# Kernel optimization log

Measured on AMD Instinct MI355X. Metric: run time of the kernel, lower is better.

Reference implementation:

```python
import jax, jax.numpy as jnp
import numpy as np

D_MODEL = 1024
HEAD_SIZE = 64

def setup_inputs() -> dict:
    key = jax.random.key(0)
    ks = jax.random.split(key, 7)
    s = 1.0 / np.sqrt(D_MODEL)
    return {
        "x": jax.random.normal(ks[0], (4, 2048, D_MODEL), dtype=jnp.float32),
        "wq": jax.random.uniform(ks[1], (D_MODEL, HEAD_SIZE), jnp.float32, -s, s),
        "bq": jax.random.uniform(ks[2], (HEAD_SIZE,), jnp.float32, -s, s),
        "wk": jax.random.uniform(ks[3], (D_MODEL, HEAD_SIZE), jnp.float32, -s, s),
        "bk": jax.random.uniform(ks[4], (HEAD_SIZE,), jnp.float32, -s, s),
        "wv": jax.random.uniform(ks[5], (D_MODEL, HEAD_SIZE), jnp.float32, -s, s),
        "bv": jax.random.uniform(ks[6], (HEAD_SIZE,), jnp.float32, -s, s),
    }

def reference(x, wq, bq, wk, bk, wv, bv):
    # x: [b, n, d_model]; projections -> [b, n, head_size]
    q = x @ wq + bq
    k = x @ wk + bk
    v = x @ wv + bv
    scores = jnp.einsum("bnd,bmd->bnm", q, k) / jnp.sqrt(jnp.float32(HEAD_SIZE))
    attn = jax.nn.softmax(scores, axis=-1)  # [b, n, n]
    return jnp.einsum("bnm,bmd->bnd", attn, v)
```

## Files before the change

kernel.cpp:

```cpp
#include <hip/hip_runtime.h>
#include <math.h>

#define D_MODEL 1024
#define HEAD 64
#define SEQ 2048
#define BATCH 4

typedef _Float16 f16x4 __attribute__((ext_vector_type(4)));
typedef _Float16 f16x8 __attribute__((ext_vector_type(8)));
typedef float f32x4 __attribute__((ext_vector_type(4)));

__global__ __launch_bounds__(256) void prep_w(
    const float* __restrict__ wq, const float* __restrict__ wk,
    const float* __restrict__ wv, _Float16* __restrict__ wT)
{
    const float* w = (blockIdx.y == 0) ? wq : (blockIdx.y == 1) ? wk : wv;
    const int kbase = blockIdx.x * 64;
    __shared__ float t[64][65];
    const int tid = threadIdx.x;
    #pragma unroll
    for (int i = 0; i < 16; i++) {
        int idx = tid + i * 256;
        int kk = idx >> 6, c = idx & 63;
        t[kk][c] = w[(size_t)(kbase + kk) * 64 + c];
    }
    __syncthreads();
    #pragma unroll
    for (int i = 0; i < 16; i++) {
        int idx = tid + i * 256;
        int c = idx >> 6, kk = idx & 63;
        wT[(size_t)(blockIdx.y * 64 + c) * 1024 + kbase + kk] = (_Float16)t[kk][c];
    }
}

__global__ __launch_bounds__(768, 6) void proj_kernel(
    const float* __restrict__ x, const _Float16* __restrict__ wT,
    const float* __restrict__ bq, const float* __restrict__ bk2,
    const float* __restrict__ bv,
    _Float16* __restrict__ q, _Float16* __restrict__ k, _Float16* __restrict__ vT)
{
    const int tid = threadIdx.x;
    const int wave = tid >> 6;
    const int lane = tid & 63;
    const int l16 = lane & 15;
    const int quad = lane >> 4;
    const int row0 = blockIdx.x * 16;

    __shared__ __align__(16) _Float16 Xs[2][16][136];

    const int srow = tid >> 5;
    const int sc4 = tid & 31;
    const float4* xg = reinterpret_cast<const float4*>(x)
                     + (size_t)(row0 + srow) * (D_MODEL / 4) + sc4;

    const _Float16* wp = wT + (size_t)(wave * 16 + l16) * D_MODEL + quad * 8;

    float4 xr;
    if (tid < 512) {
        xr = xg[0];
        f16x4 h;
        h[0] = (_Float16)xr.x; h[1] = (_Float16)xr.y;
        h[2] = (_Float16)xr.z; h[3] = (_Float16)xr.w;
        *(f16x4*)&Xs[0][srow][sc4 * 4] = h;
    }

    f32x4 acc = (f32x4){0.f, 0.f, 0.f, 0.f};

    #pragma unroll 1
    for (int c = 0; c < 8; c++) {
        __syncthreads();
        f16x8 bw0 = *(const f16x8*)(wp + c * 128);
        f16x8 bw1 = *(const f16x8*)(wp + c * 128 + 32);
        f16x8 bw2 = *(const f16x8*)(wp + c * 128 + 64);
        f16x8 bw3 = *(const f16x8*)(wp + c * 128 + 96);
        if (c < 7 && tid < 512) xr = xg[(c + 1) * 32];
        const int bsel = c & 1;
        f16x8 aX0 = *(const f16x8*)&Xs[bsel][l16][0 * 32 + quad * 8];
        f16x8 aX1 = *(const f16x8*)&Xs[bsel][l16][1 * 32 + quad * 8];
        f16x8 aX2 = *(const f16x8*)&Xs[bsel][l16][2 * 32 + quad * 8];
        f16x8 aX3 = *(const f16x8*)&Xs[bsel][l16][3 * 32 + quad * 8];
        acc = __builtin_amdgcn_mfma_f32_16x16x32_f16(aX0, bw0, acc, 0, 0, 0);
        acc = __builtin_amdgcn_mfma_f32_16x16x32_f16(aX1, bw1, acc, 0, 0, 0);
        acc = __builtin_amdgcn_mfma_f32_16x16x32_f16(aX2, bw2, acc, 0, 0, 0);
        acc = __builtin_amdgcn_mfma_f32_16x16x32_f16(aX3, bw3, acc, 0, 0, 0);
        if (c < 7 && tid < 512) {
            f16x4 h;
            h[0] = (_Float16)xr.x; h[1] = (_Float16)xr.y;
            h[2] = (_Float16)xr.z; h[3] = (_Float16)xr.w;
            *(f16x4*)&Xs[bsel ^ 1][srow][sc4 * 4] = h;
        }
    }

    const int g = wave * 16 + l16;
    const int batch = row0 / SEQ;
    const int rbase = row0 + quad * 4;
    if (g < 64) {
        float bias = bq[g];
        #pragma unroll
        for (int r = 0; r < 4; r++)
            q[(size_t)(rbase + r) * HEAD + g] = (_Float16)((acc[r] + bias) * 0.125f);
    } else if (g < 128) {
        float bias = bk2[g - 64];
        #pragma unroll
        for (int r = 0; r < 4; r++)
            k[(size_t)(rbase + r) * HEAD + (g - 64)] = (_Float16)(acc[r] + bias);
    } else {
        float bias = bv[g - 128];
        f16x4 pk;
        #pragma unroll
        for (int r = 0; r < 4; r++) pk[r] = (_Float16)(acc[r] + bias);
        const int seq0 = row0 - batch * SEQ + quad * 4;
        *(f16x4*)(vT + (size_t)(batch * HEAD + (g - 128)) * SEQ + seq0) = pk;
    }
}

__global__ __launch_bounds__(512, 4) void attn_kernel(
    const _Float16* __restrict__ q, const _Float16* __restrict__ k,
    const _Float16* __restrict__ vT, float* __restrict__ out)
{
    const int tid = threadIdx.x;
    const int wave = tid >> 6;
    const int lane = tid & 63;
    const int l16 = lane & 15;
    const int quad = lane >> 4;
    const int b = blockIdx.y;
    const int q0 = blockIdx.x * 16;

    __shared__ __align__(16) char SM[2 * 18432 + 2 * 17408];
    _Float16 (*Ks)[128][72] = (_Float16(*)[128][72])SM;
    _Float16 (*Vs)[64][136] = (_Float16(*)[64][136])(SM + 2 * 18432);
    float (*Oall)[16][68] = (float(*)[16][68])SM;
    __shared__ float Lall[8][16];

    f16x8 bQ[2];
    {
        const _Float16* qp = q + (size_t)(b * SEQ + q0 + l16) * HEAD + quad * 8;
        bQ[0] = *(const f16x8*)qp;
        bQ[1] = *(const f16x8*)(qp + 32);
    }

    f32x4 O[4];
    #pragma unroll
    for (int dt = 0; dt < 4; dt++) O[dt] = (f32x4){0.f, 0.f, 0.f, 0.f};
    float lpart = 0.f;

    const _Float16* kb = k + (size_t)b * SEQ * HEAD;
    const _Float16* vb = vT + (size_t)b * HEAD * SEQ;

    const int krow = tid >> 3, kc8 = (tid & 7) * 8;
    const int vrow = tid >> 4, vc8 = (tid & 15) * 8;
    const _Float16* kg = kb + (size_t)krow * HEAD + kc8;
    const _Float16* vg = vb + (size_t)vrow * SEQ + vc8;

    f16x8 kr0 = *(const f16x8*)kg;
    f16x8 kr1 = *(const f16x8*)(kg + (size_t)64 * HEAD);
    f16x8 vr0 = *(const f16x8*)vg;
    f16x8 vr1 = *(const f16x8*)(vg + (size_t)32 * SEQ);
    *(f16x8*)&Ks[0][krow][kc8] = kr0;
    *(f16x8*)&Ks[0][krow + 64][kc8] = kr1;
    *(f16x8*)&Vs[0][vrow][vc8] = vr0;
    *(f16x8*)&Vs[0][vrow + 32][vc8] = vr1;

    #pragma unroll 1
    for (int c = 0; c < 16; c++) {
        __syncthreads();
        if (c < 15) {
            const int kc2 = (c + 1) * 128;
            kr0 = *(const f16x8*)(kg + (size_t)kc2 * HEAD);
            kr1 = *(const f16x8*)(kg + (size_t)(kc2 + 64) * HEAD);
            vr0 = *(const f16x8*)(vg + kc2);
            vr1 = *(const f16x8*)(vg + (size_t)32 * SEQ + kc2);
        }
        const int bsel = c & 1;
        f16x8 aK0 = *(const f16x8*)&Ks[bsel][wave * 16 + l16][quad * 8];
        f16x8 aK1 = *(const f16x8*)&Ks[bsel][wave * 16 + l16][32 + quad * 8];
        f32x4 st = __builtin_amdgcn_mfma_f32_16x16x32_f16(aK0, bQ[0], (f32x4){0.f, 0.f, 0.f, 0.f}, 0, 0, 0);
        st = __builtin_amdgcn_mfma_f32_16x16x32_f16(aK1, bQ[1], st, 0, 0, 0);

        float p0 = __expf(st[0]);
        float p1 = __expf(st[1]);
        float p2 = __expf(st[2]);
        float p3 = __expf(st[3]);
        lpart += (p0 + p1) + (p2 + p3);
        f16x4 bP;
        bP[0] = (_Float16)p0; bP[1] = (_Float16)p1;
        bP[2] = (_Float16)p2; bP[3] = (_Float16)p3;

        #pragma unroll
        for (int dt = 0; dt < 4; dt++) {
            f16x4 aV = *(const f16x4*)&Vs[bsel][dt * 16 + l16][wave * 16 + quad * 4];
            O[dt] = __builtin_amdgcn_mfma_f32_16x16x16f16(aV, bP, O[dt], 0, 0, 0);
        }
        if (c < 15) {
            *(f16x8*)&Ks[bsel ^ 1][krow][kc8] = kr0;
            *(f16x8*)&Ks[bsel ^ 1][krow + 64][kc8] = kr1;
            *(f16x8*)&Vs[bsel ^ 1][vrow][vc8] = vr0;
            *(f16x8*)&Vs[bsel ^ 1][vrow + 32][vc8] = vr1;
        }
    }
    __syncthreads();

    lpart += __shfl_xor(lpart, 16);
    lpart += __shfl_xor(lpart, 32);
    if (lane < 16) Lall[wave][l16] = lpart;
    #pragma unroll
    for (int dt = 0; dt < 4; dt++)
        #pragma unroll
        for (int r = 0; r < 4; r++)
            Oall[wave][l16][dt * 16 + quad * 4 + r] = O[dt][r];
    __syncthreads();

    {
        int qi = tid >> 5;
        int dd = (tid & 31) * 2;
        float L = 0.f, o0 = 0.f, o1 = 0.f;
        #pragma unroll
        for (int w = 0; w < 8; w++) {
            L += Lall[w][qi];
            o0 += Oall[w][qi][dd];
            o1 += Oall[w][qi][dd + 1];
        }
        float inv = 1.f / L;
        float2 res = make_float2(o0 * inv, o1 * inv);
        *(float2*)(out + (size_t)(b * SEQ + q0 + qi) * HEAD + dd) = res;
    }
}

extern "C" void kernel_launch(void* const* d_in, const int* in_sizes, int n_in,
                              void* d_out, int out_size, void* d_ws, size_t ws_size,
                              hipStream_t stream) {
    const float* x  = (const float*)d_in[0];
    const float* wq = (const float*)d_in[1];
    const float* bq = (const float*)d_in[2];
    const float* wk = (const float*)d_in[3];
    const float* bk = (const float*)d_in[4];
    const float* wv = (const float*)d_in[5];
    const float* bv = (const float*)d_in[6];
    float* out = (float*)d_out;

    const size_t proj_elems = (size_t)BATCH * SEQ * HEAD;
    _Float16* qh = (_Float16*)d_ws;
    _Float16* kh = qh + proj_elems;
    _Float16* vT = kh + proj_elems;
    _Float16* wT = vT + proj_elems;

    prep_w<<<dim3(16, 3), 256, 0, stream>>>(wq, wk, wv, wT);
    proj_kernel<<<dim3(BATCH * SEQ / 16), 768, 0, stream>>>(x, wT, bq, bk, bv, qh, kh, vT);
    attn_kernel<<<dim3(SEQ / 16, BATCH), 512, 0, stream>>>(qh, kh, vT, out);
}
```

Measured before the change: 122.3 us.

## Load K/V fragments straight from global into registers, dropping LDS staging

The attention kernel no longer stages shared K and V tiles in double-buffered LDS behind per-iteration barriers. Each wave now owns a contiguous 256-key slice and loads its MFMA operand fragments directly from global memory into registers, prefetching one step ahead. The intent is to remove barrier stalls and LDS traffic and to shrink shared memory so more blocks fit per CU. The cost is narrower, less coalesced global loads (8-byte V fragments spread over many rows), which lean on L2 hits, and only a one-step prefetch to hide latency. The final O write to LDS is also vectorised.

```diff
diff --git a/kernel.cpp b/kernel.cpp
--- a/kernel.cpp
+++ b/kernel.cpp
@@ -126,56 +126,47 @@
     const int b = blockIdx.y;
     const int q0 = blockIdx.x * 16;
 
-    __shared__ __align__(16) char SM[2 * 18432 + 2 * 17408];
-    _Float16 (*Ks)[128][72] = (_Float16(*)[128][72])SM;
-    _Float16 (*Vs)[64][136] = (_Float16(*)[64][136])(SM + 2 * 18432);
-    float (*Oall)[16][68] = (float(*)[16][68])SM;
+    __shared__ __align__(16) float Oall[8][16][68];
     __shared__ float Lall[8][16];
 
-    f16x8 bQ[2];
+    f16x8 bQ0, bQ1;
     {
         const _Float16* qp = q + (size_t)(b * SEQ + q0 + l16) * HEAD + quad * 8;
-        bQ[0] = *(const f16x8*)qp;
-        bQ[1] = *(const f16x8*)(qp + 32);
-    }
+        bQ0 = *(const f16x8*)qp;
+        bQ1 = *(const f16x8*)(qp + 32);
+    }
+
+    const _Float16* kp = k + (size_t)(b * SEQ + wave * 256 + l16) * HEAD + quad * 8;
+    const _Float16* vp = vT + (size_t)(b * HEAD + l16) * SEQ + wave * 256 + quad * 4;
 
     f32x4 O[4];
     #pragma unroll
     for (int dt = 0; dt < 4; dt++) O[dt] = (f32x4){0.f, 0.f, 0.f, 0.f};
     float lpart = 0.f;
 
-    const _Float16* kb = k + (size_t)b * SEQ * HEAD;
-    const _Float16* vb = vT + (size_t)b * HEAD * SEQ;
-
-    const int krow = tid >> 3, kc8 = (tid & 7) * 8;
-    const int vrow = tid >> 4, vc8 = (tid & 15) * 8;
-    const _Float16* kg = kb + (size_t)krow * HEAD + kc8;
-    const _Float16* vg = vb + (size_t)vrow * SEQ + vc8;
-
-    f16x8 kr0 = *(const f16x8*)kg;
-    f16x8 kr1 = *(const f16x8*)(kg + (size_t)64 * HEAD);
-    f16x8 vr0 = *(const f16x8*)vg;
-    f16x8 vr1 = *(const f16x8*)(vg + (size_t)32 * SEQ);
-    *(f16x8*)&Ks[0][krow][kc8] = kr0;
-    *(f16x8*)&Ks[0][krow + 64][kc8] = kr1;
-    *(f16x8*)&Vs[0][vrow][vc8] = vr0;
-    *(f16x8*)&Vs[0][vrow + 32][vc8] = vr1;
+    f16x8 ka0 = *(const f16x8*)kp;
+    f16x8 ka1 = *(const f16x8*)(kp + 32);
+    f16x4 va0 = *(const f16x4*)vp;
+    f16x4 va1 = *(const f16x4*)(vp + 16 * SEQ);
+    f16x4 va2 = *(const f16x4*)(vp + 32 * SEQ);
+    f16x4 va3 = *(const f16x4*)(vp + 48 * SEQ);
 
     #pragma unroll 1
-    for (int c = 0; c < 16; c++) {
-        __syncthreads();
-        if (c < 15) {
-            const int kc2 = (c + 1) * 128;
-            kr0 = *(const f16x8*)(kg + (size_t)kc2 * HEAD);
-            kr1 = *(const f16x8*)(kg + (size_t)(kc2 + 64) * HEAD);
-            vr0 = *(const f16x8*)(vg + kc2);
-            vr1 = *(const f16x8*)(vg + (size_t)32 * SEQ + kc2);
-        }
-        const int bsel = c & 1;
-        f16x8 aK0 = *(const f16x8*)&Ks[bsel][wave * 16 + l16][quad * 8];
-        f16x8 aK1 = *(const f16x8*)&Ks[bsel][wave * 16 + l16][32 + quad * 8];
-        f32x4 st = __builtin_amdgcn_mfma_f32_16x16x32_f16(aK0, bQ[0], (f32x4){0.f, 0.f, 0.f, 0.f}, 0, 0, 0);
-        st = __builtin_amdgcn_mfma_f32_16x16x32_f16(aK1, bQ[1], st, 0, 0, 0);
+    for (int cc = 0; cc < 16; cc++) {
+        f16x8 nk0, nk1;
+        f16x4 nv0, nv1, nv2, nv3;
+        if (cc < 15) {
+            const _Float16* kn = kp + (size_t)(cc + 1) * 16 * HEAD;
+            nk0 = *(const f16x8*)kn;
+            nk1 = *(const f16x8*)(kn + 32);
+            const _Float16* vn = vp + (cc + 1) * 16;
+            nv0 = *(const f16x4*)vn;
+            nv1 = *(const f16x4*)(vn + 16 * SEQ);
+            nv2 = *(const f16x4*)(vn + 32 * SEQ);
+            nv3 = *(const f16x4*)(vn + 48 * SEQ);
+        }
+        f32x4 st = __builtin_amdgcn_mfma_f32_16x16x32_f16(ka0, bQ0, (f32x4){0.f, 0.f, 0.f, 0.f}, 0, 0, 0);
+        st = __builtin_amdgcn_mfma_f32_16x16x32_f16(ka1, bQ1, st, 0, 0, 0);
 
         float p0 = __expf(st[0]);
         float p1 = __expf(st[1]);
@@ -186,28 +177,23 @@
         bP[0] = (_Float16)p0; bP[1] = (_Float16)p1;
         bP[2] = (_Float16)p2; bP[3] = (_Float16)p3;
 
-        #pragma unroll
-        for (int dt = 0; dt < 4; dt++) {
-            f16x4 aV = *(const f16x4*)&Vs[bsel][dt * 16 + l16][wave * 16 + quad * 4];
-            O[dt] = __builtin_amdgcn_mfma_f32_16x16x16f16(aV, bP, O[dt], 0, 0, 0);
-        }
-        if (c < 15) {
-            *(f16x8*)&Ks[bsel ^ 1][krow][kc8] = kr0;
-            *(f16x8*)&Ks[bsel ^ 1][krow + 64][kc8] = kr1;
-            *(f16x8*)&Vs[bsel ^ 1][vrow][vc8] = vr0;
-            *(f16x8*)&Vs[bsel ^ 1][vrow + 32][vc8] = vr1;
-        }
-    }
-    __syncthreads();
+        O[0] = __builtin_amdgcn_mfma_f32_16x16x16f16(va0, bP, O[0], 0, 0, 0);
+        O[1] = __builtin_amdgcn_mfma_f32_16x16x16f16(va1, bP, O[1], 0, 0, 0);
+        O[2] = __builtin_amdgcn_mfma_f32_16x16x16f16(va2, bP, O[2], 0, 0, 0);
+        O[3] = __builtin_amdgcn_mfma_f32_16x16x16f16(va3, bP, O[3], 0, 0, 0);
+
+        if (cc < 15) {
+            ka0 = nk0; ka1 = nk1;
+            va0 = nv0; va1 = nv1; va2 = nv2; va3 = nv3;
+        }
+    }
 
     lpart += __shfl_xor(lpart, 16);
     lpart += __shfl_xor(lpart, 32);
     if (lane < 16) Lall[wave][l16] = lpart;
     #pragma unroll
     for (int dt = 0; dt < 4; dt++)
-        #pragma unroll
-        for (int r = 0; r < 4; r++)
-            Oall[wave][l16][dt * 16 + quad * 4 + r] = O[dt][r];
+        *(f32x4*)&Oall[wave][l16][dt * 16 + quad * 4] = O[dt];
     __syncthreads();
 
     {
```

After: 150.5 us. 23.1% more time.

## Share K/V tiles across two query tiles per block and pad V transpose

Applied to the files above, without the earlier changes.

The attention kernel now runs 1024 threads per block covering 32 queries, split into two 16-query groups of 8 waves. Both groups share each staged K/V chunk in LDS, so global K/V loads per query are halved and each thread issues one load per chunk instead of two. The transposed V buffer gets a padded row stride of 2080 to reduce conflicts on strided accesses. The trade-off is larger blocks with more threads synchronising on every barrier, and a larger workspace layout.

```diff
diff --git a/kernel.cpp b/kernel.cpp
--- a/kernel.cpp
+++ b/kernel.cpp
@@ -5,6 +5,7 @@
 #define HEAD 64
 #define SEQ 2048
 #define BATCH 4
+#define VSTRIDE 2080
 
 typedef _Float16 f16x4 __attribute__((ext_vector_type(4)));
 typedef _Float16 f16x8 __attribute__((ext_vector_type(8)));
@@ -110,72 +111,68 @@
         #pragma unroll
         for (int r = 0; r < 4; r++) pk[r] = (_Float16)(acc[r] + bias);
         const int seq0 = row0 - batch * SEQ + quad * 4;
-        *(f16x4*)(vT + (size_t)(batch * HEAD + (g - 128)) * SEQ + seq0) = pk;
-    }
-}
-
-__global__ __launch_bounds__(512, 4) void attn_kernel(
+        *(f16x4*)(vT + (size_t)(batch * HEAD + (g - 128)) * VSTRIDE + seq0) = pk;
+    }
+}
+
+__global__ __launch_bounds__(1024, 4) void attn_kernel(
     const _Float16* __restrict__ q, const _Float16* __restrict__ k,
     const _Float16* __restrict__ vT, float* __restrict__ out)
 {
     const int tid = threadIdx.x;
     const int wave = tid >> 6;
+    const int qt = wave >> 3;
+    const int ws = wave & 7;
     const int lane = tid & 63;
     const int l16 = lane & 15;
     const int quad = lane >> 4;
     const int b = blockIdx.y;
-    const int q0 = blockIdx.x * 16;
+    const int q0 = blockIdx.x * 32 + qt * 16;
 
     __shared__ __align__(16) char SM[2 * 18432 + 2 * 17408];
     _Float16 (*Ks)[128][72] = (_Float16(*)[128][72])SM;
     _Float16 (*Vs)[64][136] = (_Float16(*)[64][136])(SM + 2 * 18432);
     float (*Oall)[16][68] = (float(*)[16][68])SM;
-    __shared__ float Lall[8][16];
-
-    f16x8 bQ[2];
+    __shared__ float Lall[16][16];
+
+    f16x8 bQ0, bQ1;
     {
         const _Float16* qp = q + (size_t)(b * SEQ + q0 + l16) * HEAD + quad * 8;
-        bQ[0] = *(const f16x8*)qp;
-        bQ[1] = *(const f16x8*)(qp + 32);
-    }
-
-    f32x4 O[4];
-    #pragma unroll
-    for (int dt = 0; dt < 4; dt++) O[dt] = (f32x4){0.f, 0.f, 0.f, 0.f};
+        bQ0 = *(const f16x8*)qp;
+        bQ1 = *(const f16x8*)(qp + 32);
+    }
+
+    f32x4 O0 = {0.f, 0.f, 0.f, 0.f};
+    f32x4 O1 = {0.f, 0.f, 0.f, 0.f};
+    f32x4 O2 = {0.f, 0.f, 0.f, 0.f};
+    f32x4 O3 = {0.f, 0.f, 0.f, 0.f};
     float lpart = 0.f;
 
     const _Float16* kb = k + (size_t)b * SEQ * HEAD;
-    const _Float16* vb = vT + (size_t)b * HEAD * SEQ;
+    const _Float16* vb = vT + (size_t)b * HEAD * VSTRIDE;
 
     const int krow = tid >> 3, kc8 = (tid & 7) * 8;
     const int vrow = tid >> 4, vc8 = (tid & 15) * 8;
     const _Float16* kg = kb + (size_t)krow * HEAD + kc8;
-    const _Float16* vg = vb + (size_t)vrow * SEQ + vc8;
-
-    f16x8 kr0 = *(const f16x8*)kg;
-    f16x8 kr1 = *(const f16x8*)(kg + (size_t)64 * HEAD);
-    f16x8 vr0 = *(const f16x8*)vg;
-    f16x8 vr1 = *(const f16x8*)(vg + (size_t)32 * SEQ);
-    *(f16x8*)&Ks[0][krow][kc8] = kr0;
-    *(f16x8*)&Ks[0][krow + 64][kc8] = kr1;
-    *(f16x8*)&Vs[0][vrow][vc8] = vr0;
-    *(f16x8*)&Vs[0][vrow + 32][vc8] = vr1;
+    const _Float16* vg = vb + (size_t)vrow * VSTRIDE + vc8;
+
+    f16x8 kr = *(const f16x8*)kg;
+    f16x8 vr = *(const f16x8*)vg;
+    *(f16x8*)&Ks[0][krow][kc8] = kr;
+    *(f16x8*)&Vs[0][vrow][vc8] = vr;
 
     #pragma unroll 1
     for (int c = 0; c < 16; c++) {
         __syncthreads();
         if (c < 15) {
-            const int kc2 = (c + 1) * 128;
-            kr0 = *(const f16x8*)(kg + (size_t)kc2 * HEAD);
-            kr1 = *(const f16x8*)(kg + (size_t)(kc2 + 64) * HEAD);
-            vr0 = *(const f16x8*)(vg + kc2);
-            vr1 = *(const f16x8*)(vg + (size_t)32 * SEQ + kc2);
+            kr = *(const f16x8*)(kg + (size_t)(c + 1) * 128 * HEAD);
+            vr = *(const f16x8*)(vg + (c + 1) * 128);
         }
         const int bsel = c & 1;
-        f16x8 aK0 = *(const f16x8*)&Ks[bsel][wave * 16 + l16][quad * 8];
-        f16x8 aK1 = *(const f16x8*)&Ks[bsel][wave * 16 + l16][32 + quad * 8];
-        f32x4 st = __builtin_amdgcn_mfma_f32_16x16x32_f16(aK0, bQ[0], (f32x4){0.f, 0.f, 0.f, 0.f}, 0, 0, 0);
-        st = __builtin_amdgcn_mfma_f32_16x16x32_f16(aK1, bQ[1], st, 0, 0, 0);
+        f16x8 aK0 = *(const f16x8*)&Ks[bsel][ws * 16 + l16][quad * 8];
+        f16x8 aK1 = *(const f16x8*)&Ks[bsel][ws * 16 + l16][32 + quad * 8];
+        f32x4 st = __builtin_amdgcn_mfma_f32_16x16x32_f16(aK0, bQ0, (f32x4){0.f, 0.f, 0.f, 0.f}, 0, 0, 0);
+        st = __builtin_amdgcn_mfma_f32_16x16x32_f16(aK1, bQ1, st, 0, 0, 0);
 
         float p0 = __expf(st[0]);
         float p1 = __expf(st[1]);
@@ -186,16 +183,18 @@
         bP[0] = (_Float16)p0; bP[1] = (_Float16)p1;
         bP[2] = (_Float16)p2; bP[3] = (_Float16)p3;
 
-        #pragma unroll
-        for (int dt = 0; dt < 4; dt++) {
-            f16x4 aV = *(const f16x4*)&Vs[bsel][dt * 16 + l16][wave * 16 + quad * 4];
-            O[dt] = __builtin_amdgcn_mfma_f32_16x16x16f16(aV, bP, O[dt], 0, 0, 0);
-        }
+        f16x4 aV0 = *(const f16x4*)&Vs[bsel][0 * 16 + l16][ws * 16 + quad * 4];
+        f16x4 aV1 = *(const f16x4*)&Vs[bsel][1 * 16 + l16][ws * 16 + quad * 4];
+        f16x4 aV2 = *(const f16x4*)&Vs[bsel][2 * 16 + l16][ws * 16 + quad * 4];
+        f16x4 aV3 = *(const f16x4*)&Vs[bsel][3 * 16 + l16][ws * 16 + quad * 4];
+        O0 = __builtin_amdgcn_mfma_f32_16x16x16f16(aV0, bP, O0, 0, 0, 0);
+        O1 = __builtin_amdgcn_mfma_f32_16x16x16f16(aV1, bP, O1, 0, 0, 0);
+        O2 = __builtin_amdgcn_mfma_f32_16x16x16f16(aV2, bP, O2, 0, 0, 0);
+        O3 = __builtin_amdgcn_mfma_f32_16x16x16f16(aV3, bP, O3, 0, 0, 0);
+
         if (c < 15) {
-            *(f16x8*)&Ks[bsel ^ 1][krow][kc8] = kr0;
-            *(f16x8*)&Ks[bsel ^ 1][krow + 64][kc8] = kr1;
-            *(f16x8*)&Vs[bsel ^ 1][vrow][vc8] = vr0;
-            *(f16x8*)&Vs[bsel ^ 1][vrow + 32][vc8] = vr1;
+            *(f16x8*)&Ks[bsel ^ 1][krow][kc8] = kr;
+            *(f16x8*)&Vs[bsel ^ 1][vrow][vc8] = vr;
         }
     }
     __syncthreads();
@@ -203,26 +202,27 @@
     lpart += __shfl_xor(lpart, 16);
     lpart += __shfl_xor(lpart, 32);
     if (lane < 16) Lall[wave][l16] = lpart;
-    #pragma unroll
-    for (int dt = 0; dt < 4; dt++)
-        #pragma unroll
-        for (int r = 0; r < 4; r++)
-            Oall[wave][l16][dt * 16 + quad * 4 + r] = O[dt][r];
+    *(f32x4*)&Oall[wave][l16][0 * 16 + quad * 4] = O0;
+    *(f32x4*)&Oall[wave][l16][1 * 16 + quad * 4] = O1;
+    *(f32x4*)&Oall[wave][l16][2 * 16 + quad * 4] = O2;
+    *(f32x4*)&Oall[wave][l16][3 * 16 + quad * 4] = O3;
     __syncthreads();
 
     {
         int qi = tid >> 5;
         int dd = (tid & 31) * 2;
+        int wbase = (qi >> 4) * 8;
+        int qr = qi & 15;
         float L = 0.f, o0 = 0.f, o1 = 0.f;
         #pragma unroll
         for (int w = 0; w < 8; w++) {
-            L += Lall[w][qi];
-            o0 += Oall[w][qi][dd];
-            o1 += Oall[w][qi][dd + 1];
+            L += Lall[wbase + w][qr];
+            o0 += Oall[wbase + w][qr][dd];
+            o1 += Oall[wbase + w][qr][dd + 1];
         }
         float inv = 1.f / L;
         float2 res = make_float2(o0 * inv, o1 * inv);
-        *(float2*)(out + (size_t)(b * SEQ + q0 + qi) * HEAD + dd) = res;
+        *(float2*)(out + (size_t)(b * SEQ + blockIdx.x * 32 + qi) * HEAD + dd) = res;
     }
 }
 
@@ -242,9 +242,9 @@
     _Float16* qh = (_Float16*)d_ws;
     _Float16* kh = qh + proj_elems;
     _Float16* vT = kh + proj_elems;
-    _Float16* wT = vT + proj_elems;
+    _Float16* wT = vT + (size_t)BATCH * HEAD * VSTRIDE;
 
     prep_w<<<dim3(16, 3), 256, 0, stream>>>(wq, wk, wv, wT);
     proj_kernel<<<dim3(BATCH * SEQ / 16), 768, 0, stream>>>(x, wT, bq, bk, bv, qh, kh, vT);
-    attn_kernel<<<dim3(SEQ / 16, BATCH), 512, 0, stream>>>(qh, kh, vT, out);
-}
+    attn_kernel<<<dim3(SEQ / 32, BATCH), 1024, 0, stream>>>(qh, kh, vT, out);
+}
```

Result: no change. 121.8 us (-0.4%).

## Give each wave private KV slices and process 32 queries per block

Applied to the files above, without the earlier changes.

The attention kernel now handles 32 query rows per block and reuses each K and V fragment across two query tiles. Each wave streams its own contiguous range of 256 keys into a private double-buffered LDS region, which removes the per-iteration block-wide barrier. The V projection output is re-laid out into 16-key tiles so each wave reads V contiguously, and the K tile in LDS uses an XOR swizzle to avoid bank conflicts. This costs more LDS per block (about 68KB) and more accumulator registers, and the launch-bounds occupancy hint is dropped, so fewer blocks may be resident per CU.

```diff
diff --git a/kernel.cpp b/kernel.cpp
--- a/kernel.cpp
+++ b/kernel.cpp
@@ -110,11 +110,12 @@
         #pragma unroll
         for (int r = 0; r < 4; r++) pk[r] = (_Float16)(acc[r] + bias);
         const int seq0 = row0 - batch * SEQ + quad * 4;
-        *(f16x4*)(vT + (size_t)(batch * HEAD + (g - 128)) * SEQ + seq0) = pk;
-    }
-}
-
-__global__ __launch_bounds__(512, 4) void attn_kernel(
+        const int d = g - 128;
+        *(f16x4*)(vT + ((size_t)(batch * 128 + (seq0 >> 4)) * 64 + d) * 16 + (seq0 & 15)) = pk;
+    }
+}
+
+__global__ __launch_bounds__(512) void attn_kernel(
     const _Float16* __restrict__ q, const _Float16* __restrict__ k,
     const _Float16* __restrict__ vT, float* __restrict__ out)
 {
@@ -124,105 +125,123 @@
     const int l16 = lane & 15;
     const int quad = lane >> 4;
     const int b = blockIdx.y;
-    const int q0 = blockIdx.x * 16;
-
-    __shared__ __align__(16) char SM[2 * 18432 + 2 * 17408];
-    _Float16 (*Ks)[128][72] = (_Float16(*)[128][72])SM;
-    _Float16 (*Vs)[64][136] = (_Float16(*)[64][136])(SM + 2 * 18432);
-    float (*Oall)[16][68] = (float(*)[16][68])SM;
-    __shared__ float Lall[8][16];
-
-    f16x8 bQ[2];
+    const int q0 = blockIdx.x * 32;
+
+    __shared__ __align__(16) char SM[69632];
+    _Float16* KV = (_Float16*)SM;
+    float (*Oall)[2][16][68] = (float(*)[2][16][68])SM;
+    __shared__ float Lall[8][2][16];
+
+    const int wb = wave * 4096;
+
+    f16x8 bQ00, bQ01, bQ10, bQ11;
     {
         const _Float16* qp = q + (size_t)(b * SEQ + q0 + l16) * HEAD + quad * 8;
-        bQ[0] = *(const f16x8*)qp;
-        bQ[1] = *(const f16x8*)(qp + 32);
-    }
-
-    f32x4 O[4];
-    #pragma unroll
-    for (int dt = 0; dt < 4; dt++) O[dt] = (f32x4){0.f, 0.f, 0.f, 0.f};
-    float lpart = 0.f;
-
-    const _Float16* kb = k + (size_t)b * SEQ * HEAD;
-    const _Float16* vb = vT + (size_t)b * HEAD * SEQ;
-
-    const int krow = tid >> 3, kc8 = (tid & 7) * 8;
-    const int vrow = tid >> 4, vc8 = (tid & 15) * 8;
-    const _Float16* kg = kb + (size_t)krow * HEAD + kc8;
-    const _Float16* vg = vb + (size_t)vrow * SEQ + vc8;
-
-    f16x8 kr0 = *(const f16x8*)kg;
-    f16x8 kr1 = *(const f16x8*)(kg + (size_t)64 * HEAD);
-    f16x8 vr0 = *(const f16x8*)vg;
-    f16x8 vr1 = *(const f16x8*)(vg + (size_t)32 * SEQ);
-    *(f16x8*)&Ks[0][krow][kc8] = kr0;
-    *(f16x8*)&Ks[0][krow + 64][kc8] = kr1;
-    *(f16x8*)&Vs[0][vrow][vc8] = vr0;
-    *(f16x8*)&Vs[0][vrow + 32][vc8] = vr1;
+        bQ00 = *(const f16x8*)qp;
+        bQ01 = *(const f16x8*)(qp + 32);
+        bQ10 = *(const f16x8*)(qp + 16 * HEAD);
+        bQ11 = *(const f16x8*)(qp + 16 * HEAD + 32);
+    }
+
+    const _Float16* kgb = k + (size_t)(b * SEQ + wave * 256) * HEAD + lane * 8;
+    const _Float16* vgb = vT + (size_t)(b * 128 + wave * 16) * 1024 + lane * 8;
+
+    const int kw = (lane >> 3) * 64 + (((lane & 7) ^ (lane >> 3)) * 8);
+    const int vw = lane * 8;
+
+    f32x4 O0[4], O1[4];
+    #pragma unroll
+    for (int dt = 0; dt < 4; dt++) {
+        O0[dt] = (f32x4){0.f, 0.f, 0.f, 0.f};
+        O1[dt] = (f32x4){0.f, 0.f, 0.f, 0.f};
+    }
+    float lp0 = 0.f, lp1 = 0.f;
+
+    f16x8 kr0 = *(const f16x8*)kgb;
+    f16x8 kr1 = *(const f16x8*)(kgb + 512);
+    f16x8 vr0 = *(const f16x8*)vgb;
+    f16x8 vr1 = *(const f16x8*)(vgb + 512);
+    *(f16x8*)&KV[wb + kw] = kr0;
+    *(f16x8*)&KV[wb + kw + 512] = kr1;
+    *(f16x8*)&KV[wb + 2048 + vw] = vr0;
+    *(f16x8*)&KV[wb + 2048 + vw + 512] = vr1;
 
     #pragma unroll 1
     for (int c = 0; c < 16; c++) {
-        __syncthreads();
         if (c < 15) {
-            const int kc2 = (c + 1) * 128;
-            kr0 = *(const f16x8*)(kg + (size_t)kc2 * HEAD);
-            kr1 = *(const f16x8*)(kg + (size_t)(kc2 + 64) * HEAD);
-            vr0 = *(const f16x8*)(vg + kc2);
-            vr1 = *(const f16x8*)(vg + (size_t)32 * SEQ + kc2);
+            kr0 = *(const f16x8*)(kgb + (c + 1) * 1024);
+            kr1 = *(const f16x8*)(kgb + (c + 1) * 1024 + 512);
+            vr0 = *(const f16x8*)(vgb + (c + 1) * 1024);
+            vr1 = *(const f16x8*)(vgb + (c + 1) * 1024 + 512);
         }
         const int bsel = c & 1;
-        f16x8 aK0 = *(const f16x8*)&Ks[bsel][wave * 16 + l16][quad * 8];
-        f16x8 aK1 = *(const f16x8*)&Ks[bsel][wave * 16 + l16][32 + quad * 8];
-        f32x4 st = __builtin_amdgcn_mfma_f32_16x16x32_f16(aK0, bQ[0], (f32x4){0.f, 0.f, 0.f, 0.f}, 0, 0, 0);
-        st = __builtin_amdgcn_mfma_f32_16x16x32_f16(aK1, bQ[1], st, 0, 0, 0);
-
-        float p0 = __expf(st[0]);
-        float p1 = __expf(st[1]);
-        float p2 = __expf(st[2]);
-        float p3 = __expf(st[3]);
-        lpart += (p0 + p1) + (p2 + p3);
-        f16x4 bP;
-        bP[0] = (_Float16)p0; bP[1] = (_Float16)p1;
-        bP[2] = (_Float16)p2; bP[3] = (_Float16)p3;
+        const _Float16* Kl = KV + wb + bsel * 1024;
+        const _Float16* Vl = KV + wb + 2048 + bsel * 1024;
+        f16x8 aK0 = *(const f16x8*)&Kl[l16 * 64 + ((quad ^ (l16 & 7)) * 8)];
+        f16x8 aK1 = *(const f16x8*)&Kl[l16 * 64 + (((quad + 4) ^ (l16 & 7)) * 8)];
+        f32x4 s0 = __builtin_amdgcn_mfma_f32_16x16x32_f16(aK0, bQ00, (f32x4){0.f, 0.f, 0.f, 0.f}, 0, 0, 0);
+        s0 = __builtin_amdgcn_mfma_f32_16x16x32_f16(aK1, bQ01, s0, 0, 0, 0);
+        f32x4 s1 = __builtin_amdgcn_mfma_f32_16x16x32_f16(aK0, bQ10, (f32x4){0.f, 0.f, 0.f, 0.f}, 0, 0, 0);
+        s1 = __builtin_amdgcn_mfma_f32_16x16x32_f16(aK1, bQ11, s1, 0, 0, 0);
+
+        float p00 = __expf(s0[0]), p01 = __expf(s0[1]);
+        float p02 = __expf(s0[2]), p03 = __expf(s0[3]);
+        float p10 = __expf(s1[0]), p11 = __expf(s1[1]);
+        float p12 = __expf(s1[2]), p13 = __expf(s1[3]);
+        lp0 += (p00 + p01) + (p02 + p03);
+        lp1 += (p10 + p11) + (p12 + p13);
+        f16x4 bP0, bP1;
+        bP0[0] = (_Float16)p00; bP0[1] = (_Float16)p01;
+        bP0[2] = (_Float16)p02; bP0[3] = (_Float16)p03;
+        bP1[0] = (_Float16)p10; bP1[1] = (_Float16)p11;
+        bP1[2] = (_Float16)p12; bP1[3] = (_Float16)p13;
 
         #pragma unroll
         for (int dt = 0; dt < 4; dt++) {
-            f16x4 aV = *(const f16x4*)&Vs[bsel][dt * 16 + l16][wave * 16 + quad * 4];
-            O[dt] = __builtin_amdgcn_mfma_f32_16x16x16f16(aV, bP, O[dt], 0, 0, 0);
-        }
+            f16x4 aV = *(const f16x4*)&Vl[(dt * 16 + l16) * 16 + quad * 4];
+            O0[dt] = __builtin_amdgcn_mfma_f32_16x16x16f16(aV, bP0, O0[dt], 0, 0, 0);
+            O1[dt] = __builtin_amdgcn_mfma_f32_16x16x16f16(aV, bP1, O1[dt], 0, 0, 0);
+        }
+
         if (c < 15) {
-            *(f16x8*)&Ks[bsel ^ 1][krow][kc8] = kr0;
-            *(f16x8*)&Ks[bsel ^ 1][krow + 64][kc8] = kr1;
-            *(f16x8*)&Vs[bsel ^ 1][vrow][vc8] = vr0;
-            *(f16x8*)&Vs[bsel ^ 1][vrow + 32][vc8] = vr1;
-        }
-    }
+            const int nsel = bsel ^ 1;
+            *(f16x8*)&KV[wb + nsel * 1024 + kw] = kr0;
+            *(f16x8*)&KV[wb + nsel * 1024 + kw + 512] = kr1;
+            *(f16x8*)&KV[wb + 2048 + nsel * 1024 + vw] = vr0;
+            *(f16x8*)&KV[wb + 2048 + nsel * 1024 + vw + 512] = vr1;
+        }
+    }
+
+    lp0 += __shfl_xor(lp0, 16);
+    lp0 += __shfl_xor(lp0, 32);
+    lp1 += __shfl_xor(lp1, 16);
+    lp1 += __shfl_xor(lp1, 32);
     __syncthreads();
-
-    lpart += __shfl_xor(lpart, 16);
-    lpart += __shfl_xor(lpart, 32);
-    if (lane < 16) Lall[wave][l16] = lpart;
-    #pragma unroll
-    for (int dt = 0; dt < 4; dt++)
-        #pragma unroll
-        for (int r = 0; r < 4; r++)
-            Oall[wave][l16][dt * 16 + quad * 4 + r] = O[dt][r];
+    if (lane < 16) {
+        Lall[wave][0][l16] = lp0;
+        Lall[wave][1][l16] = lp1;
+    }
+    #pragma unroll
+    for (int dt = 0; dt < 4; dt++) {
+        *(f32x4*)&Oall[wave][0][l16][dt * 16 + quad * 4] = O0[dt];
+        *(f32x4*)&Oall[wave][1][l16][dt * 16 + quad * 4] = O1[dt];
+    }
     __syncthreads();
 
     {
-        int qi = tid >> 5;
-        int dd = (tid & 31) * 2;
-        float L = 0.f, o0 = 0.f, o1 = 0.f;
+        int qi = tid >> 4;
+        int dd = (tid & 15) * 4;
+        int t = qi >> 4, q16 = qi & 15;
+        float L = 0.f, a0 = 0.f, a1 = 0.f, a2 = 0.f, a3 = 0.f;
         #pragma unroll
         for (int w = 0; w < 8; w++) {
-            L += Lall[w][qi];
-            o0 += Oall[w][qi][dd];
-            o1 += Oall[w][qi][dd + 1];
+            L += Lall[w][t][q16];
+            const float* op = &Oall[w][t][q16][dd];
+            a0 += op[0]; a1 += op[1]; a2 += op[2]; a3 += op[3];
         }
         float inv = 1.f / L;
-        float2 res = make_float2(o0 * inv, o1 * inv);
-        *(float2*)(out + (size_t)(b * SEQ + q0 + qi) * HEAD + dd) = res;
+        float4 res = make_float4(a0 * inv, a1 * inv, a2 * inv, a3 * inv);
+        *(float4*)(out + (size_t)(b * SEQ + q0 + qi) * HEAD + dd) = res;
     }
 }
 
@@ -246,5 +265,5 @@
 
     prep_w<<<dim3(16, 3), 256, 0, stream>>>(wq, wk, wv, wT);
     proj_kernel<<<dim3(BATCH * SEQ / 16), 768, 0, stream>>>(x, wT, bq, bk, bv, qh, kh, vT);
-    attn_kernel<<<dim3(SEQ / 16, BATCH), 512, 0, stream>>>(qh, kh, vT, out);
-}
+    attn_kernel<<<dim3(SEQ / 32, BATCH), 512, 0, stream>>>(qh, kh, vT, out);
+}
```

Measured after the change: 117.4 us. 3.9% less time.
